# Optimization experiments

Measured on AMD Instinct MI355X. Metric: run time of the kernel, lower is better.

## Reference

```python
import jax, jax.numpy as jnp
import numpy as np

B, N, D, H, LH, AH = 4, 2048, 512, 4, 64, 64
NUM_BUCKETS = 128
EPS = 1e-6
LENGTHS = np.array([2048, 1536, 1024, 1792])  # jagged per-sequence lengths, sum = 6400


def _ln(x, eps=EPS):
    # F.layer_norm without affine params (biased variance)
    m = jnp.mean(x, axis=-1, keepdims=True)
    v = jnp.var(x, axis=-1, keepdims=True)
    return (x - m) * jax.lax.rsqrt(v + eps)


def _rel_bias(all_timestamps, ts_w):
    # bucketed time-delta relative attention bias -> [B, N, N]
    delta = (all_timestamps[:, :, None] - all_timestamps[:, None, :]).astype(jnp.float32)
    bucket = jnp.clip(jnp.floor(jnp.log1p(jnp.abs(delta))).astype(jnp.int32), 0, NUM_BUCKETS)
    return ts_w[bucket]


def setup_inputs() -> dict:
    key = jax.random.key(0)
    ks = jax.random.split(key, 6)
    offsets = np.concatenate([[0], np.cumsum(LENGTHS)]).astype(np.int32)
    T = int(offsets[-1])
    token_batch = np.repeat(np.arange(B), LENGTHS).astype(np.int32)
    token_pos = np.concatenate([np.arange(l) for l in LENGTHS]).astype(np.int32)
    x = jax.random.normal(ks[0], (T, D), jnp.float32)
    uvqk = jax.random.normal(ks[1], (D, 2 * LH * H + 2 * AH * H), jnp.float32) * 0.02
    o_w = jax.random.normal(ks[2], (D, LH * H), jnp.float32) * 0.02  # torch Linear weight [out, in]
    o_b = jnp.zeros((D,), jnp.float32)
    ts_w = jax.random.normal(ks[3], (NUM_BUCKETS + 1,), jnp.float32) * 0.02
    all_timestamps = jnp.sort(jax.random.randint(ks[4], (B, N), 0, 1000000, jnp.int32), axis=-1)
    invalid_attn_mask = jnp.tril(jnp.ones((N, N), jnp.float32))  # causal validity mask in {0,1}
    return {
        'x': x, 'uvqk': uvqk, 'o_w': o_w, 'o_b': o_b, 'ts_w': ts_w,
        'all_timestamps': all_timestamps, 'invalid_attn_mask': invalid_attn_mask,
        'x_offsets': jnp.asarray(offsets), 'token_batch': jnp.asarray(token_batch),
        'token_pos': jnp.asarray(token_pos),
    }


def reference(x, uvqk, o_w, o_b, ts_w, all_timestamps, invalid_attn_mask,
              x_offsets, token_batch, token_pos):
    # input layernorm + fused uvqk projection with SiLU
    h = jax.nn.silu(_ln(x) @ uvqk)  # [T, 2*H*LH + 2*H*AH]
    u, v, q, k = jnp.split(h, [LH * H, 2 * LH * H, 2 * LH * H + AH * H], axis=1)

    def pad(vals):  # jagged [T, d] -> padded dense [B, N, d]
        return jnp.zeros((B, N, vals.shape[-1]), vals.dtype).at[token_batch, token_pos].set(vals)

    pq = pad(q).reshape(B, N, H, AH)
    pk = pad(k).reshape(B, N, H, AH)
    pv = pad(v).reshape(B, N, H, LH)

    scores = jnp.einsum('bnhd,bmhd->bhnm', pq, pk)
    scores = scores + _rel_bias(all_timestamps, ts_w)[:, None]  # broadcast over heads
    scores = jax.nn.silu(scores) / N
    scores = scores * invalid_attn_mask[None, None]
    attn = jnp.einsum('bhnm,bmhd->bnhd', scores, pv).reshape(B, N, H * LH)
    attn_j = attn[token_batch, token_pos]  # dense -> jagged [T, H*LH]

    o_in = u * _ln(attn_j)
    return o_in @ o_w.T + o_b + x
```

## Files before the change

### kernel.cpp

```cpp
#include <hip/hip_runtime.h>
#include <math.h>


typedef __attribute__((ext_vector_type(8))) short bf16x8;
typedef __attribute__((ext_vector_type(4))) float f32x4;
typedef __attribute__((ext_vector_type(2))) unsigned int u32x2;
typedef __attribute__((ext_vector_type(4))) unsigned int u32x4;

__device__ __forceinline__ float silu_over_2048(float v) {
    return v * __builtin_amdgcn_rcpf(2048.0f + 2048.0f * __expf(-v));
}

__device__ __forceinline__ float silu_f(float v) {
    return v * __builtin_amdgcn_rcpf(1.0f + __expf(-v));
}

__device__ __forceinline__ unsigned short f2bf(float f) {
    unsigned int u = __float_as_uint(f);
    u += 0x7fffu + ((u >> 16) & 1u);
    return (unsigned short)(u >> 16);
}

__device__ __forceinline__ unsigned int f2bf2(float lo, float hi) {
#if __has_builtin(__builtin_amdgcn_cvt_pk_bf16_f32)
    typedef __attribute__((ext_vector_type(2))) short bf16x2;
    bf16x2 p = __builtin_amdgcn_cvt_pk_bf16_f32(lo, hi);
    return *(unsigned int*)&p;
#else
    return (unsigned int)f2bf(lo) | ((unsigned int)f2bf(hi) << 16);
#endif
}

__device__ __forceinline__ void gload_lds16(const unsigned short* g, unsigned short* l) {
    __builtin_amdgcn_global_load_lds(
        (const __attribute__((address_space(1))) void*)(g),
        (__attribute__((address_space(3))) void*)(l),
        16, 0, 0);
}

__global__ __launch_bounds__(256) void k1_ln_prep(const float* __restrict__ x,
                                                  unsigned short* __restrict__ xnb,
                                                  const float* __restrict__ uvqk,
                                                  unsigned short* __restrict__ uvqkT,
                                                  const float* __restrict__ ow,
                                                  unsigned short* __restrict__ owb) {
    const int tid = threadIdx.x;
    const int bx = blockIdx.x;
    if (bx < 1600) {
        const int row = bx * 4 + (tid >> 6);
        const int lane = tid & 63;
        const float* xr = x + row * 512 + lane * 8;
        const float4 v0 = *(const float4*)xr;
        const float4 v1 = *(const float4*)(xr + 4);
        float s = v0.x + v0.y + v0.z + v0.w + v1.x + v1.y + v1.z + v1.w;
        float ss = v0.x * v0.x + v0.y * v0.y + v0.z * v0.z + v0.w * v0.w +
                   v1.x * v1.x + v1.y * v1.y + v1.z * v1.z + v1.w * v1.w;
#pragma unroll
        for (int off = 32; off > 0; off >>= 1) {
            s += __shfl_down(s, off);
            ss += __shfl_down(ss, off);
        }
        s = __shfl(s, 0);
        ss = __shfl(ss, 0);
        const float mean = s * (1.0f / 512.0f);
        const float var = ss * (1.0f / 512.0f) - mean * mean;
        const float rstd = rsqrtf(var + 1e-6f);
        unsigned int pk[4];
        pk[0] = f2bf2((v0.x - mean) * rstd, (v0.y - mean) * rstd);
        pk[1] = f2bf2((v0.z - mean) * rstd, (v0.w - mean) * rstd);
        pk[2] = f2bf2((v1.x - mean) * rstd, (v1.y - mean) * rstd);
        pk[3] = f2bf2((v1.z - mean) * rstd, (v1.w - mean) * rstd);
        *(uint4*)(xnb + row * 512 + lane * 8) = *(const uint4*)pk;
    } else if (bx < 1728) {
        __shared__ float L[64][68];
        const int t = bx - 1600;
        const int n0 = (t & 15) * 64;
        const int k0 = (t >> 4) * 64;
#pragma unroll
        for (int i = 0; i < 4; ++i) {
            const int r = (tid >> 4) + i * 16;
            const int c = (tid & 15) * 4;
            *(float4*)&L[r][c] = *(const float4*)(uvqk + (k0 + r) * 1024 + n0 + c);
        }
        __syncthreads();
        const int n = tid >> 2;
        const int kb = (tid & 3) * 16;
#pragma unroll
        for (int pass = 0; pass < 2; ++pass) {
            unsigned short pk[8];
#pragma unroll
            for (int j = 0; j < 8; ++j) pk[j] = f2bf(L[kb + pass * 8 + j][n]);
            *(uint4*)(uvqkT + (n0 + n) * 512 + k0 + kb + pass * 8) = *(const uint4*)pk;
        }
    } else {
        const int base = ((bx - 1728) * 256 + tid) * 8;
        float4 a = *(const float4*)(ow + base);
        float4 b = *(const float4*)(ow + base + 4);
        unsigned short pk[8] = {f2bf(a.x), f2bf(a.y), f2bf(a.z), f2bf(a.w),
                                f2bf(b.x), f2bf(b.y), f2bf(b.z), f2bf(b.w)};
        *(uint4*)(owb + base) = *(const uint4*)pk;
    }
}

__global__ __launch_bounds__(256, 4) void k2_gemm1(const unsigned short* __restrict__ A,
                                                   const unsigned short* __restrict__ Bt,
                                                   unsigned short* __restrict__ u_out,
                                                   unsigned short* __restrict__ hb,
                                                   unsigned short* __restrict__ vtb) {
    __shared__ __align__(16) unsigned short smem[12288];
    unsigned short* As = smem;
    unsigned short* Bs0 = smem + 4096;
    unsigned short* Bs1 = smem + 8192;
    const int tid = threadIdx.x;
    const int lane = tid & 63;
    const int w = tid >> 6;
    const int l15 = lane & 15;
    const int quad = lane >> 4;
    const int bid = blockIdx.x;
    const int kk_ = (bid & 7) * 100 + (bid >> 3);
    const int bm = (kk_ >> 3) * 64;
    const int bn0 = (kk_ & 7) * 128;

    const int srow = lane >> 3;
    const int scol = ((lane & 7) ^ srow) * 8;
    const unsigned short* gA = A + (size_t)(bm + w * 8 + srow) * 512 + scol;
    const unsigned short* gB0 = Bt + (size_t)(bn0 + w * 8 + srow) * 512 + scol;
    const unsigned short* gB1 = Bt + (size_t)(bn0 + 64 + w * 8 + srow) * 512 + scol;

    const int xA = (l15 & 7) << 3;
    f32x4 acc[2][4] = {};
    for (int kc = 0; kc < 512; kc += 64) {
        __syncthreads();
#pragma unroll
        for (int i = 0; i < 2; ++i) {
            gload_lds16(gA + (size_t)(i * 32) * 512 + kc, As + (w + i * 4) * 512);
            gload_lds16(gB0 + (size_t)(i * 32) * 512 + kc, Bs0 + (w + i * 4) * 512);
            gload_lds16(gB1 + (size_t)(i * 32) * 512 + kc, Bs1 + (w + i * 4) * 512);
        }
        __syncthreads();
        const bf16x8 a0 = *(const bf16x8*)&As[(w * 16 + l15) * 64 + ((quad * 8) ^ xA)];
        const bf16x8 a1 = *(const bf16x8*)&As[(w * 16 + l15) * 64 + ((32 + quad * 8) ^ xA)];
#pragma unroll
        for (int nt = 0; nt < 4; ++nt) {
            bf16x8 b0 = *(const bf16x8*)&Bs0[(nt * 16 + l15) * 64 + ((quad * 8) ^ xA)];
            bf16x8 b1 = *(const bf16x8*)&Bs0[(nt * 16 + l15) * 64 + ((32 + quad * 8) ^ xA)];
            acc[0][nt] = __builtin_amdgcn_mfma_f32_16x16x32_bf16(a0, b0, acc[0][nt], 0, 0, 0);
            acc[0][nt] = __builtin_amdgcn_mfma_f32_16x16x32_bf16(a1, b1, acc[0][nt], 0, 0, 0);
        }
#pragma unroll
        for (int nt = 0; nt < 4; ++nt) {
            bf16x8 b0 = *(const bf16x8*)&Bs1[(nt * 16 + l15) * 64 + ((quad * 8) ^ xA)];
            bf16x8 b1 = *(const bf16x8*)&Bs1[(nt * 16 + l15) * 64 + ((32 + quad * 8) ^ xA)];
            acc[1][nt] = __builtin_amdgcn_mfma_f32_16x16x32_bf16(a0, b0, acc[1][nt], 0, 0, 0);
            acc[1][nt] = __builtin_amdgcn_mfma_f32_16x16x32_bf16(a1, b1, acc[1][nt], 0, 0, 0);
        }
    }
    const int m = bm + w * 16 + quad * 4;
    unsigned short(*T)[72] = (unsigned short(*)[72])smem;
    if (bn0 < 256) {
#pragma unroll
        for (int p = 0; p < 2; ++p) {
            __syncthreads();
#pragma unroll
            for (int nt = 0; nt < 4; ++nt) {
                unsigned int p01 = f2bf2(silu_f(acc[p][nt][0]), silu_f(acc[p][nt][1]));
                unsigned int p23 = f2bf2(silu_f(acc[p][nt][2]), silu_f(acc[p][nt][3]));
                T[w * 16 + quad * 4 + 0][nt * 16 + l15] = (unsigned short)p01;
                T[w * 16 + quad * 4 + 1][nt * 16 + l15] = (unsigned short)(p01 >> 16);
                T[w * 16 + quad * 4 + 2][nt * 16 + l15] = (unsigned short)p23;
                T[w * 16 + quad * 4 + 3][nt * 16 + l15] = (unsigned short)(p23 >> 16);
            }
            __syncthreads();
            const int sr = tid >> 3, sc2 = (tid & 7) * 8;
#pragma unroll
            for (int i = 0; i < 2; ++i) {
                const int r = sr + i * 32;
                __builtin_nontemporal_store(
                    *(const u32x4*)&T[r][sc2],
                    (u32x4*)(u_out + (size_t)(bm + r) * 256 + bn0 + p * 64 + sc2));
            }
        }
    } else if (bn0 < 512) {
#pragma unroll
        for (int p = 0; p < 2; ++p) {
            __syncthreads();
#pragma unroll
            for (int nt = 0; nt < 4; ++nt) {
                unsigned int p01 = f2bf2(silu_f(acc[p][nt][0]), silu_f(acc[p][nt][1]));
                unsigned int p23 = f2bf2(silu_f(acc[p][nt][2]), silu_f(acc[p][nt][3]));
                unsigned int pk2[2] = {p01, p23};
                *(uint2*)&T[nt * 16 + l15][w * 16 + quad * 4] = *(const uint2*)pk2;
            }
            __syncthreads();
            const int sr = tid >> 3, sc2 = (tid & 7) * 8;
#pragma unroll
            for (int i = 0; i < 2; ++i) {
                const int r = sr + i * 32;
                *(uint4*)(vtb + (size_t)(bn0 - 256 + p * 64 + r) * 6400 + bm + sc2) =
                    *(const uint4*)&T[r][sc2];
            }
        }
    } else {
#pragma unroll
        for (int p = 0; p < 2; ++p) {
            __syncthreads();
#pragma unroll
            for (int nt = 0; nt < 4; ++nt) {
                unsigned int p01 = f2bf2(silu_f(acc[p][nt][0]), silu_f(acc[p][nt][1]));
                unsigned int p23 = f2bf2(silu_f(acc[p][nt][2]), silu_f(acc[p][nt][3]));
                T[w * 16 + quad * 4 + 0][nt * 16 + l15] = (unsigned short)p01;
                T[w * 16 + quad * 4 + 1][nt * 16 + l15] = (unsigned short)(p01 >> 16);
                T[w * 16 + quad * 4 + 2][nt * 16 + l15] = (unsigned short)p23;
                T[w * 16 + quad * 4 + 3][nt * 16 + l15] = (unsigned short)(p23 >> 16);
            }
            __syncthreads();
            const int sr = tid >> 3, sc2 = (tid & 7) * 8;
#pragma unroll
            for (int i = 0; i < 2; ++i) {
                const int r = sr + i * 32;
                *(uint4*)(hb + (size_t)(bm + r) * 768 + (bn0 - 256) + p * 64 + sc2) =
                    *(const uint4*)&T[r][sc2];
            }
        }
    }
}

__global__ __launch_bounds__(256, 5) void k3_attn(const unsigned short* __restrict__ hb,
                                                  const unsigned short* __restrict__ vtb,
                                                  const int* __restrict__ ts,
                                                  const float* __restrict__ tsw,
                                                  const int* __restrict__ offs,
                                                  unsigned short* __restrict__ part) {
    const int xcd = blockIdx.x & 7;
    const int slot = blockIdx.x >> 3;
    const int b = (xcd < 3) ? 0 : (xcd < 5) ? 1 : (xcd == 5) ? 2 : 3;
    const int xst = (b == 0) ? 0 : (b == 1) ? 3 : (b == 2) ? 5 : 6;
    const int kx = (b == 0) ? 3 : (b == 2) ? 1 : 2;
    const int r = slot * kx + (xcd - xst);
    const int off = offs[b];
    const int len = offs[b + 1] - off;
    const int nqt = len >> 6;
    const int qt_lpt = r >> 5;
    if (qt_lpt >= nqt) return;
    const int qt = nqt - 1 - qt_lpt;
    const int c = (r >> 2) & 7;
    const int hd = r & 3;
    if (c * 4 > qt) return;
    const int q0 = qt * 64;
    const int kt_lo = c * 4;
    const int kt_hi = min(qt, c * 4 + 3);

    __shared__ __align__(16) unsigned short QPs[64][72];
    __shared__ __align__(16) unsigned short Ks[4096];
    __shared__ __align__(16) unsigned short Vt[4096];
    __shared__ float tqf[64], tkf[64];
    __shared__ float tw[132];

    const int tid = threadIdx.x;
    const int lane = tid & 63;
    const int w = tid >> 6;
    const int l15 = lane & 15;
    const int quad = lane >> 4;
    const int sr = tid >> 3;
    const int sc = (tid & 7) * 8;

    const int srow = lane >> 3;
    const int scol = ((lane & 7) ^ srow) * 8;
    const int xA = (l15 & 7) << 3;

    if (tid < 129) tw[tid] = tsw[tid];
    if (tid < 64) tqf[tid] = (float)ts[b * 2048 + q0 + tid];
#pragma unroll
    for (int i = 0; i < 2; ++i)
        *(uint4*)&QPs[sr + i * 32][sc] =
            *(const uint4*)(hb + (off + q0 + sr + i * 32) * 768 + 256 + hd * 64 + sc);
    __syncthreads();

    const bf16x8 aQ0 = *(const bf16x8*)&QPs[w * 16 + l15][quad * 8];
    const bf16x8 aQ1 = *(const bf16x8*)&QPs[w * 16 + l15][32 + quad * 8];
    const f32x4 tq4 = *(const f32x4*)&tqf[w * 16 + quad * 4];
    const int nbase = q0 + w * 16 + quad * 4;

    const unsigned short* gK = hb + (size_t)(off + w * 8 + srow) * 768 + 512 + hd * 64 + scol;
    const unsigned short* gV = vtb + (size_t)(hd * 64 + w * 8 + srow) * 6400 + off + scol;

    f32x4 oacc[4] = {};

    for (int kt = kt_lo; kt <= kt_hi; ++kt) {
        const int m0 = kt * 64;
        __syncthreads();
#pragma unroll
        for (int i = 0; i < 2; ++i) {
            gload_lds16(gK + (size_t)(m0 + i * 32) * 768, Ks + (w + i * 4) * 512);
            gload_lds16(gV + (size_t)(i * 32) * 6400 + m0, Vt + (w + i * 4) * 512);
        }
        if (tid < 64) tkf[tid] = (float)ts[b * 2048 + m0 + tid];
        __syncthreads();

        f32x4 s[4] = {};
#pragma unroll
        for (int nt = 0; nt < 4; ++nt) {
            bf16x8 b0 = *(const bf16x8*)&Ks[(nt * 16 + l15) * 64 + ((quad * 8) ^ xA)];
            bf16x8 b1 = *(const bf16x8*)&Ks[(nt * 16 + l15) * 64 + ((32 + quad * 8) ^ xA)];
            s[nt] = __builtin_amdgcn_mfma_f32_16x16x32_bf16(aQ0, b0, s[nt], 0, 0, 0);
            s[nt] = __builtin_amdgcn_mfma_f32_16x16x32_bf16(aQ1, b1, s[nt], 0, 0, 0);
        }

        const bool diag = (kt == qt);
#pragma unroll
        for (int nt = 0; nt < 4; ++nt) {
            const int m = m0 + nt * 16 + l15;
            const float tk = tkf[nt * 16 + l15];
            float p[4];
#pragma unroll
            for (int reg = 0; reg < 4; ++reg) {
                const float delta = fabsf(tq4[reg] - tk);
                const int bucket = (int)(__log2f(1.0f + delta) * 0.6931471805599453f);
                float val = s[nt][reg] + tw[bucket];
                float pv = silu_over_2048(val);
                if (diag) pv = (m <= nbase + reg) ? pv : 0.0f;
                p[reg] = pv;
            }
            const unsigned int p01 = f2bf2(p[0], p[1]);
            const unsigned int p23 = f2bf2(p[2], p[3]);
            QPs[w * 16 + quad * 4 + 0][nt * 16 + l15] = (unsigned short)p01;
            QPs[w * 16 + quad * 4 + 1][nt * 16 + l15] = (unsigned short)(p01 >> 16);
            QPs[w * 16 + quad * 4 + 2][nt * 16 + l15] = (unsigned short)p23;
            QPs[w * 16 + quad * 4 + 3][nt * 16 + l15] = (unsigned short)(p23 >> 16);
        }

        const bf16x8 aP0 = *(const bf16x8*)&QPs[w * 16 + l15][quad * 8];
        const bf16x8 aP1 = *(const bf16x8*)&QPs[w * 16 + l15][32 + quad * 8];
#pragma unroll
        for (int nt = 0; nt < 4; ++nt) {
            bf16x8 v0 = *(const bf16x8*)&Vt[(nt * 16 + l15) * 64 + ((quad * 8) ^ xA)];
            bf16x8 v1 = *(const bf16x8*)&Vt[(nt * 16 + l15) * 64 + ((32 + quad * 8) ^ xA)];
            oacc[nt] = __builtin_amdgcn_mfma_f32_16x16x32_bf16(aP0, v0, oacc[nt], 0, 0, 0);
            oacc[nt] = __builtin_amdgcn_mfma_f32_16x16x32_bf16(aP1, v1, oacc[nt], 0, 0, 0);
        }
    }

    unsigned short* pc = part + (size_t)c * (6400 * 256);
#pragma unroll
    for (int nt = 0; nt < 4; ++nt)
#pragma unroll
        for (int reg = 0; reg < 4; ++reg)
            __builtin_nontemporal_store(
                f2bf(oacc[nt][reg]),
                &pc[(off + q0 + w * 16 + quad * 4 + reg) * 256 + hd * 64 + nt * 16 + l15]);
}

__global__ __launch_bounds__(256) void k4a_ln(const unsigned short* __restrict__ part,
                                              const unsigned short* __restrict__ u_in,
                                              const int* __restrict__ token_pos,
                                              unsigned short* __restrict__ o_in) {
    const int row = blockIdx.x * 4 + (threadIdx.x >> 6);
    const int lane = threadIdx.x & 63;
    const int qt = token_pos[row] >> 6;
    const int nch = (qt + 4) >> 2;
    const size_t base = (size_t)row * 256 + lane * 4;
    float a0 = 0.0f, a1 = 0.0f, a2 = 0.0f, a3 = 0.0f;
    for (int cc = 0; cc < nch; ++cc) {
        const u32x2 pw =
            __builtin_nontemporal_load((const u32x2*)(part + (size_t)cc * (6400 * 256) + base));
        a0 += __uint_as_float(pw[0] << 16);
        a1 += __uint_as_float(pw[0] & 0xffff0000u);
        a2 += __uint_as_float(pw[1] << 16);
        a3 += __uint_as_float(pw[1] & 0xffff0000u);
    }
    float s = a0 + a1 + a2 + a3;
    float ss = a0 * a0 + a1 * a1 + a2 * a2 + a3 * a3;
#pragma unroll
    for (int off = 32; off > 0; off >>= 1) {
        s += __shfl_down(s, off);
        ss += __shfl_down(ss, off);
    }
    s = __shfl(s, 0);
    ss = __shfl(ss, 0);
    const float mean = s * (1.0f / 256.0f);
    const float var = ss * (1.0f / 256.0f) - mean * mean;
    const float rstd = rsqrtf(var + 1e-6f);
    const u32x2 uw = __builtin_nontemporal_load((const u32x2*)(u_in + base));
    const float u0 = __uint_as_float(uw[0] << 16);
    const float u1 = __uint_as_float(uw[0] & 0xffff0000u);
    const float u2 = __uint_as_float(uw[1] << 16);
    const float u3 = __uint_as_float(uw[1] & 0xffff0000u);
    unsigned int pk[2];
    pk[0] = f2bf2(u0 * (a0 - mean) * rstd, u1 * (a1 - mean) * rstd);
    pk[1] = f2bf2(u2 * (a2 - mean) * rstd, u3 * (a3 - mean) * rstd);
    *(uint2*)(o_in + base) = *(const uint2*)pk;
}

__global__ __launch_bounds__(256, 4) void k4b_gemm2(const unsigned short* __restrict__ A,
                                                    const unsigned short* __restrict__ owb,
                                                    const float* __restrict__ ob,
                                                    const float* __restrict__ x,
                                                    float* __restrict__ out) {
    __shared__ __align__(16) unsigned short smem[8192];
    unsigned short* As = smem;
    unsigned short* Bs = smem + 4096;
    const int tid = threadIdx.x;
    const int lane = tid & 63;
    const int w = tid >> 6;
    const int l15 = lane & 15;
    const int quad = lane >> 4;
    const int bid = blockIdx.x;
    const int kk_ = (bid & 7) * 100 + (bid >> 3);
    const int bm = (kk_ >> 3) * 64;
    const int bn = (kk_ & 7) * 64;

    const int srow = lane >> 3;
    const int scol = ((lane & 7) ^ srow) * 8;
    const unsigned short* gA = A + (size_t)(bm + w * 8 + srow) * 256 + scol;
    const unsigned short* gB = owb + (size_t)(bn + w * 8 + srow) * 256 + scol;

    const int xA = (l15 & 7) << 3;
    f32x4 acc[4] = {};
    for (int kc = 0; kc < 256; kc += 64) {
        __syncthreads();
#pragma unroll
        for (int i = 0; i < 2; ++i) {
            gload_lds16(gA + (size_t)(i * 32) * 256 + kc, As + (w + i * 4) * 512);
            gload_lds16(gB + (size_t)(i * 32) * 256 + kc, Bs + (w + i * 4) * 512);
        }
        __syncthreads();
        const bf16x8 a0 = *(const bf16x8*)&As[(w * 16 + l15) * 64 + ((quad * 8) ^ xA)];
        const bf16x8 a1 = *(const bf16x8*)&As[(w * 16 + l15) * 64 + ((32 + quad * 8) ^ xA)];
#pragma unroll
        for (int nt = 0; nt < 4; ++nt) {
            bf16x8 b0 = *(const bf16x8*)&Bs[(nt * 16 + l15) * 64 + ((quad * 8) ^ xA)];
            bf16x8 b1 = *(const bf16x8*)&Bs[(nt * 16 + l15) * 64 + ((32 + quad * 8) ^ xA)];
            acc[nt] = __builtin_amdgcn_mfma_f32_16x16x32_bf16(a0, b0, acc[nt], 0, 0, 0);
            acc[nt] = __builtin_amdgcn_mfma_f32_16x16x32_bf16(a1, b1, acc[nt], 0, 0, 0);
        }
    }
    const int m = bm + w * 16 + quad * 4;
#pragma unroll
    for (int nt = 0; nt < 4; ++nt) {
        const int d = bn + nt * 16 + l15;
        const float bias = ob[d];
#pragma unroll
        for (int reg = 0; reg < 4; ++reg)
            out[(m + reg) * 512 + d] = acc[nt][reg] + bias + x[(m + reg) * 512 + d];
    }
}

extern "C" void kernel_launch(void* const* d_in, const int* in_sizes, int n_in,
                              void* d_out, int out_size, void* d_ws, size_t ws_size,
                              hipStream_t stream) {
    const float* x = (const float*)d_in[0];
    const float* uvqk = (const float*)d_in[1];
    const float* ow = (const float*)d_in[2];
    const float* ob = (const float*)d_in[3];
    const float* tsw = (const float*)d_in[4];
    const int* ts = (const int*)d_in[5];
    const int* offs = (const int*)d_in[7];
    const int* token_pos = (const int*)d_in[9];
    float* out = (float*)d_out;

    unsigned short* u = (unsigned short*)d_ws;
    unsigned short* part = u + 6400 * 256;
    unsigned short* xnb = part + 8 * 6400 * 256;
    unsigned short* hb = xnb + 6400 * 512;
    unsigned short* o_in = hb + 6400 * 768;
    unsigned short* uvqkT = o_in + 6400 * 256;
    unsigned short* owb = uvqkT + 1024 * 512;
    unsigned short* vtb = owb + 512 * 256;

    k1_ln_prep<<<1792, 256, 0, stream>>>(x, xnb, uvqk, uvqkT, ow, owb);
    k2_gemm1<<<800, 256, 0, stream>>>(xnb, uvqkT, u, hb, vtb);
    k3_attn<<<4096, 256, 0, stream>>>(hb, vtb, ts, tsw, offs, part);
    k4a_ln<<<1600, 256, 0, stream>>>(part, u, token_pos, o_in);
    k4b_gemm2<<<800, 256, 0, stream>>>(o_in, owb, ob, x, out);
}
```

Baseline: 146.8 us.

## Double-buffer LDS tiles in both projection GEMM kernels

Both GEMM kernels now use two LDS buffers per operand. Each iteration issues the async global-to-LDS load for the next K chunk before running the MFMAs on the current one, and the two barriers per iteration become one. The aim is to hide global load latency behind matrix math. The cost is double the LDS footprint, so the first GEMM's launch bound drops from 4 to 3 blocks per CU, which may lower occupancy.

Measured after the change: 148.2 us. About the same (+0.9%).

```diff
diff --git a/kernel.cpp b/kernel.cpp
--- a/kernel.cpp
+++ b/kernel.cpp
@@ -102,15 +102,12 @@
     }
 }
 
-__global__ __launch_bounds__(256, 4) void k2_gemm1(const unsigned short* __restrict__ A,
+__global__ __launch_bounds__(256, 3) void k2_gemm1(const unsigned short* __restrict__ A,
                                                    const unsigned short* __restrict__ Bt,
                                                    unsigned short* __restrict__ u_out,
                                                    unsigned short* __restrict__ hb,
                                                    unsigned short* __restrict__ vtb) {
-    __shared__ __align__(16) unsigned short smem[12288];
-    unsigned short* As = smem;
-    unsigned short* Bs0 = smem + 4096;
-    unsigned short* Bs1 = smem + 8192;
+    __shared__ __align__(16) unsigned short smem[24576];
     const int tid = threadIdx.x;
     const int lane = tid & 63;
     const int w = tid >> 6;
@@ -127,19 +124,27 @@
     const unsigned short* gB0 = Bt + (size_t)(bn0 + w * 8 + srow) * 512 + scol;
     const unsigned short* gB1 = Bt + (size_t)(bn0 + 64 + w * 8 + srow) * 512 + scol;
 
+    auto stage = [&](int kc, unsigned short* base) {
+#pragma unroll
+        for (int i = 0; i < 2; ++i) {
+            gload_lds16(gA + (size_t)(i * 32) * 512 + kc, base + (w + i * 4) * 512);
+            gload_lds16(gB0 + (size_t)(i * 32) * 512 + kc, base + 4096 + (w + i * 4) * 512);
+            gload_lds16(gB1 + (size_t)(i * 32) * 512 + kc, base + 8192 + (w + i * 4) * 512);
+        }
+    };
+
     const int xA = (l15 & 7) << 3;
     f32x4 acc[2][4] = {};
-    for (int kc = 0; kc < 512; kc += 64) {
-        __syncthreads();
-#pragma unroll
-        for (int i = 0; i < 2; ++i) {
-            gload_lds16(gA + (size_t)(i * 32) * 512 + kc, As + (w + i * 4) * 512);
-            gload_lds16(gB0 + (size_t)(i * 32) * 512 + kc, Bs0 + (w + i * 4) * 512);
-            gload_lds16(gB1 + (size_t)(i * 32) * 512 + kc, Bs1 + (w + i * 4) * 512);
-        }
-        __syncthreads();
-        const bf16x8 a0 = *(const bf16x8*)&As[(w * 16 + l15) * 64 + ((quad * 8) ^ xA)];
-        const bf16x8 a1 = *(const bf16x8*)&As[(w * 16 + l15) * 64 + ((32 + quad * 8) ^ xA)];
+    stage(0, smem);
+    __syncthreads();
+#pragma unroll
+    for (int it = 0; it < 8; ++it) {
+        unsigned short* cb = smem + (it & 1) * 12288;
+        if (it < 7) stage((it + 1) * 64, smem + ((it + 1) & 1) * 12288);
+        const unsigned short* Bs0 = cb + 4096;
+        const unsigned short* Bs1 = cb + 8192;
+        const bf16x8 a0 = *(const bf16x8*)&cb[(w * 16 + l15) * 64 + ((quad * 8) ^ xA)];
+        const bf16x8 a1 = *(const bf16x8*)&cb[(w * 16 + l15) * 64 + ((32 + quad * 8) ^ xA)];
 #pragma unroll
         for (int nt = 0; nt < 4; ++nt) {
             bf16x8 b0 = *(const bf16x8*)&Bs0[(nt * 16 + l15) * 64 + ((quad * 8) ^ xA)];
@@ -154,6 +159,7 @@
             acc[1][nt] = __builtin_amdgcn_mfma_f32_16x16x32_bf16(a0, b0, acc[1][nt], 0, 0, 0);
             acc[1][nt] = __builtin_amdgcn_mfma_f32_16x16x32_bf16(a1, b1, acc[1][nt], 0, 0, 0);
         }
+        __syncthreads();
     }
     const int m = bm + w * 16 + quad * 4;
     unsigned short(*T)[72] = (unsigned short(*)[72])smem;
@@ -396,9 +402,7 @@
                                                     const float* __restrict__ ob,
                                                     const float* __restrict__ x,
                                                     float* __restrict__ out) {
-    __shared__ __align__(16) unsigned short smem[8192];
-    unsigned short* As = smem;
-    unsigned short* Bs = smem + 4096;
+    __shared__ __align__(16) unsigned short smem[16384];
     const int tid = threadIdx.x;
     const int lane = tid & 63;
     const int w = tid >> 6;
@@ -414,18 +418,25 @@
     const unsigned short* gA = A + (size_t)(bm + w * 8 + srow) * 256 + scol;
     const unsigned short* gB = owb + (size_t)(bn + w * 8 + srow) * 256 + scol;
 
+    auto stage = [&](int kc, unsigned short* base) {
+#pragma unroll
+        for (int i = 0; i < 2; ++i) {
+            gload_lds16(gA + (size_t)(i * 32) * 256 + kc, base + (w + i * 4) * 512);
+            gload_lds16(gB + (size_t)(i * 32) * 256 + kc, base + 4096 + (w + i * 4) * 512);
+        }
+    };
+
     const int xA = (l15 & 7) << 3;
     f32x4 acc[4] = {};
-    for (int kc = 0; kc < 256; kc += 64) {
-        __syncthreads();
-#pragma unroll
-        for (int i = 0; i < 2; ++i) {
-            gload_lds16(gA + (size_t)(i * 32) * 256 + kc, As + (w + i * 4) * 512);
-            gload_lds16(gB + (size_t)(i * 32) * 256 + kc, Bs + (w + i * 4) * 512);
-        }
-        __syncthreads();
-        const bf16x8 a0 = *(const bf16x8*)&As[(w * 16 + l15) * 64 + ((quad * 8) ^ xA)];
-        const bf16x8 a1 = *(const bf16x8*)&As[(w * 16 + l15) * 64 + ((32 + quad * 8) ^ xA)];
+    stage(0, smem);
+    __syncthreads();
+#pragma unroll
+    for (int it = 0; it < 4; ++it) {
+        unsigned short* cb = smem + (it & 1) * 8192;
+        if (it < 3) stage((it + 1) * 64, smem + ((it + 1) & 1) * 8192);
+        const unsigned short* Bs = cb + 4096;
+        const bf16x8 a0 = *(const bf16x8*)&cb[(w * 16 + l15) * 64 + ((quad * 8) ^ xA)];
+        const bf16x8 a1 = *(const bf16x8*)&cb[(w * 16 + l15) * 64 + ((32 + quad * 8) ^ xA)];
 #pragma unroll
         for (int nt = 0; nt < 4; ++nt) {
             bf16x8 b0 = *(const bf16x8*)&Bs[(nt * 16 + l15) * 64 + ((quad * 8) ^ xA)];
@@ -433,6 +444,7 @@
             acc[nt] = __builtin_amdgcn_mfma_f32_16x16x32_bf16(a0, b0, acc[nt], 0, 0, 0);
             acc[nt] = __builtin_amdgcn_mfma_f32_16x16x32_bf16(a1, b1, acc[nt], 0, 0, 0);
         }
+        __syncthreads();
     }
     const int m = bm + w * 16 + quad * 4;
 #pragma unroll
```
